# Kernel tuning notes

Measured on AMD Instinct MI355X. Metric: run time of the kernel, lower is better.

## Reference

```python
import jax, jax.numpy as jnp
import numpy as np

D_MODEL = 1024
N_HEADS = 16
HEAD_DIM = D_MODEL // N_HEADS


def setup_inputs() -> dict:
    key = jax.random.key(0)
    ks = jax.random.split(key, 5)
    x = jax.random.normal(ks[0], (4, 2048, D_MODEL), dtype=jnp.float32)
    # Linear weights stored torch-style as (out, in); biases (out,)
    s = 1.0 / np.sqrt(D_MODEL)
    W_qkv = jax.random.uniform(ks[1], (3 * D_MODEL, D_MODEL), jnp.float32, -s, s)
    b_qkv = jax.random.uniform(ks[2], (3 * D_MODEL,), jnp.float32, -s, s)
    W_proj = jax.random.uniform(ks[3], (D_MODEL, D_MODEL), jnp.float32, -s, s)
    b_proj = jax.random.uniform(ks[4], (D_MODEL,), jnp.float32, -s, s)
    return {"x": x, "W_qkv": W_qkv, "b_qkv": b_qkv, "W_proj": W_proj, "b_proj": b_proj}


def reference(x, W_qkv, b_qkv, W_proj, b_proj):
    B, T, C = x.shape
    nh, hs = N_HEADS, HEAD_DIM
    qkv = jnp.einsum('btc,oc->bto', x, W_qkv) + b_qkv  # (B,T,3C)
    q, k, v = jnp.split(qkv, 3, axis=-1)
    # (B, nh, T, hs)
    q = q.reshape(B, T, nh, hs).transpose(0, 2, 1, 3)
    k = k.reshape(B, T, nh, hs).transpose(0, 2, 1, 3)
    v = v.reshape(B, T, nh, hs).transpose(0, 2, 1, 3)
    att = jnp.einsum('bhqd,bhkd->bhqk', q, k) * (hs ** -0.5)  # (B,nh,T,T)
    causal = jnp.tril(jnp.ones((T, T), dtype=bool))
    att = jnp.where(causal[None, None], att, -jnp.inf)
    att = jax.nn.softmax(att, axis=-1)
    y = jnp.einsum('bhqk,bhkd->bhqd', att, v)  # (B,nh,T,hs)
    y = y.transpose(0, 2, 1, 3).reshape(B, T, C)
    y = jnp.einsum('btc,oc->bto', y, W_proj) + b_proj
    return y
```

## Files before the change

kernel.cpp:

```cpp
#include <hip/hip_runtime.h>
#include <math.h>

typedef __bf16 bf16;
typedef __bf16 bf16x4 __attribute__((ext_vector_type(4)));
typedef __bf16 bf16x8 __attribute__((ext_vector_type(8)));
typedef float  f32x4  __attribute__((ext_vector_type(4)));
typedef unsigned short u16;

#define MFMA16(a, b, c) __builtin_amdgcn_mfma_f32_16x16x32_bf16((a), (b), (c), 0, 0, 0)

constexpr int Bz    = 4;
constexpr int Ts    = 2048;
constexpr int DM    = 1024;
constexpr int NH    = 16;
constexpr int HS    = 64;
constexpr int MROWS = Bz * Ts;
constexpr int NQKV  = 3 * DM;

__device__ __forceinline__ unsigned int pack2(bf16 lo, bf16 hi) {
    return ((unsigned int)__builtin_bit_cast(u16, hi) << 16) |
            (unsigned int)__builtin_bit_cast(u16, lo);
}

__device__ __forceinline__ void load_lds16(const bf16* g, bf16* l) {
    __builtin_amdgcn_global_load_lds(
        (__attribute__((address_space(1))) void*)(g),
        (__attribute__((address_space(3))) void*)(l), 16, 0, 0);
}

__global__ void cvt_kernel(const float* __restrict__ in, bf16* __restrict__ out, int n4) {
    int i = blockIdx.x * blockDim.x + threadIdx.x;
    if (i < n4) {
        float4 v = ((const float4*)in)[i];
        bf16x4 o = { (bf16)v.x, (bf16)v.y, (bf16)v.z, (bf16)v.w };
        ((bf16x4*)out)[i] = o;
    }
}

template <int OUT_BF16>
__global__ __launch_bounds__(256) void gemm_bt(const bf16* __restrict__ A,
                                               const bf16* __restrict__ Bw,
                                               const float* __restrict__ bias,
                                               void* __restrict__ Cout,
                                               int M, int N, int K)
{
    __shared__ __align__(16) bf16 As[128 * 32];
    __shared__ __align__(16) bf16 Bs[128 * 32];

    const int tid  = threadIdx.x;
    const int wave = tid >> 6, lane = tid & 63;
    const int quad = lane >> 4, l16 = lane & 15;
    const int wm = (wave >> 1) * 64, wn = (wave & 1) * 64;
    const int m0 = blockIdx.x * 128, n0 = blockIdx.y * 128;

    f32x4 acc[4][4] = {};

    const int c0 = tid, c1 = tid + 256;
    const bf16* gA0 = A  + (size_t)(m0 + (c0 >> 2)) * K + (c0 & 3) * 8;
    const bf16* gA1 = A  + (size_t)(m0 + (c1 >> 2)) * K + (c1 & 3) * 8;
    const bf16* gB0 = Bw + (size_t)(n0 + (c0 >> 2)) * K + (c0 & 3) * 8;
    const bf16* gB1 = Bw + (size_t)(n0 + (c1 >> 2)) * K + (c1 & 3) * 8;
    bf16* lA0 = As + c0 * 8;  bf16* lA1 = As + c1 * 8;
    bf16* lB0 = Bs + c0 * 8;  bf16* lB1 = Bs + c1 * 8;

    for (int kb = 0; kb < K; kb += 32) {
        if (kb) __syncthreads();
        load_lds16(gA0 + kb, lA0);
        load_lds16(gA1 + kb, lA1);
        load_lds16(gB0 + kb, lB0);
        load_lds16(gB1 + kb, lB1);
        __syncthreads();

        bf16x8 af[4], bfr[4];
#pragma unroll
        for (int mt = 0; mt < 4; ++mt)
            af[mt] = *(const bf16x8*)(As + (wm + mt * 16 + l16) * 32 + quad * 8);
#pragma unroll
        for (int nt = 0; nt < 4; ++nt)
            bfr[nt] = *(const bf16x8*)(Bs + (wn + nt * 16 + l16) * 32 + quad * 8);
#pragma unroll
        for (int mt = 0; mt < 4; ++mt)
#pragma unroll
            for (int nt = 0; nt < 4; ++nt)
                acc[mt][nt] = MFMA16(af[mt], bfr[nt], acc[mt][nt]);
    }

#pragma unroll
    for (int mt = 0; mt < 4; ++mt)
#pragma unroll
        for (int nt = 0; nt < 4; ++nt) {
            const int row = m0 + wm + mt * 16 + quad * 4;
            const int col = n0 + wn + nt * 16 + l16;
            const float bc = bias[col];
#pragma unroll
            for (int r = 0; r < 4; ++r) {
                const float v = acc[mt][nt][r] + bc;
                if (OUT_BF16) ((bf16*)Cout)[(size_t)(row + r) * N + col] = (bf16)v;
                else          ((float*)Cout)[(size_t)(row + r) * N + col] = v;
            }
        }
}

__device__ __forceinline__ int vswz(int d) { return ((d ^ (d >> 3)) & 7) << 3; }

__global__ __launch_bounds__(256) void attn_kernel(const bf16* __restrict__ qkv,
                                                   bf16* __restrict__ y)
{
    __shared__ __align__(16) bf16 Ks[64][72];
    __shared__ __align__(16) bf16 Vt[64][72];
    __shared__ __align__(16) bf16 Ps[4][16][72];

    const int p = blockIdx.x, h = blockIdx.y, b = blockIdx.z;
    const int tid  = threadIdx.x;
    const int wave = tid >> 6, lane = tid & 63;
    const int quad = lane >> 4, l16 = lane & 15;

    const bf16* kbase = qkv + (size_t)(b * Ts) * NQKV + DM     + h * HS;
    const bf16* vbase = qkv + (size_t)(b * Ts) * NQKV + 2 * DM + h * HS;

    const int dg = tid & 7, kp = tid >> 3;
    const int k0 = 2 * kp;

    for (int phase = 0; phase < 2; ++phase) {
        const int qt = phase ? (31 - p) : p;
        const int qw = qt * 64 + wave * 16;
        const int q_abs = qw + l16;

        const bf16* qrow = qkv + (size_t)(b * Ts + qw + l16) * NQKV + h * HS;
        const bf16x8 qf0 = *(const bf16x8*)(qrow + quad * 8);
        const bf16x8 qf1 = *(const bf16x8*)(qrow + 32 + quad * 8);

        f32x4 o[4] = {};
        float m_run = -1e30f, l_run = 0.f;

        for (int kt = 0; kt <= qt; ++kt) {
            __syncthreads();

            {
                int e = tid * 8;
#pragma unroll
                for (int rr = 0; rr < 2; ++rr, e += 2048) {
                    const int key = e >> 6, c = e & 63;
                    bf16x8 kv = *(const bf16x8*)(kbase + (size_t)(kt * 64 + key) * NQKV + c);
                    *(bf16x8*)&Ks[key][c] = kv;
                }
            }
            {
                const bf16x8 v0 = *(const bf16x8*)(vbase + (size_t)(kt * 64 + k0)     * NQKV + dg * 8);
                const bf16x8 v1 = *(const bf16x8*)(vbase + (size_t)(kt * 64 + k0 + 1) * NQKV + dg * 8);
#pragma unroll
                for (int j = 0; j < 8; ++j) {
                    const int d = dg * 8 + j;
                    *(unsigned int*)&Vt[d][k0 ^ vswz(d)] = pack2(v0[j], v1[j]);
                }
            }
            __syncthreads();

            f32x4 s[4];
#pragma unroll
            for (int sub = 0; sub < 4; ++sub) {
                bf16x8 kf0 = *(const bf16x8*)&Ks[sub * 16 + l16][quad * 8];
                bf16x8 kf1 = *(const bf16x8*)&Ks[sub * 16 + l16][32 + quad * 8];
                f32x4 z = {};
                z = MFMA16(kf0, qf0, z);
                z = MFMA16(kf1, qf1, z);
                s[sub] = z;
            }

#pragma unroll
            for (int sub = 0; sub < 4; ++sub) {
                const int kb = kt * 64 + sub * 16 + quad * 4;
#pragma unroll
                for (int r = 0; r < 4; ++r)
                    s[sub][r] = (kb + r <= q_abs) ? s[sub][r] * 0.125f : -1e30f;
            }

            float mx = -1e30f;
#pragma unroll
            for (int sub = 0; sub < 4; ++sub)
#pragma unroll
                for (int r = 0; r < 4; ++r) mx = fmaxf(mx, s[sub][r]);
            mx = fmaxf(mx, __shfl_xor(mx, 16, 64));
            mx = fmaxf(mx, __shfl_xor(mx, 32, 64));
            const float mnew  = fmaxf(m_run, mx);
            const float alpha = __expf(m_run - mnew);
            float ls = 0.f;
#pragma unroll
            for (int sub = 0; sub < 4; ++sub)
#pragma unroll
                for (int r = 0; r < 4; ++r) {
                    const float pv = __expf(s[sub][r] - mnew);
                    s[sub][r] = pv;
                    ls += pv;
                }
            ls += __shfl_xor(ls, 16, 64);
            ls += __shfl_xor(ls, 32, 64);
            l_run = l_run * alpha + ls;
            m_run = mnew;
#pragma unroll
            for (int dt = 0; dt < 4; ++dt)
#pragma unroll
                for (int r = 0; r < 4; ++r) o[dt][r] *= alpha;

#pragma unroll
            for (int sub = 0; sub < 4; ++sub) {
                const int kc = sub * 16 + quad * 4;
                *(unsigned int*)&Ps[wave][l16][kc]     = pack2((bf16)s[sub][0], (bf16)s[sub][1]);
                *(unsigned int*)&Ps[wave][l16][kc + 2] = pack2((bf16)s[sub][2], (bf16)s[sub][3]);
            }
            __asm__ volatile("" ::: "memory");

            bf16x8 pb0 = *(const bf16x8*)&Ps[wave][l16][quad * 8];
            bf16x8 pb1 = *(const bf16x8*)&Ps[wave][l16][32 + quad * 8];

#pragma unroll
            for (int kb = 0; kb < 2; ++kb) {
                const int kcol = kb * 32 + quad * 8;
#pragma unroll
                for (int dt = 0; dt < 4; ++dt) {
                    const int d = dt * 16 + l16;
                    bf16x8 vf = *(const bf16x8*)&Vt[d][kcol ^ vswz(d)];
                    o[dt] = MFMA16(vf, kb ? pb1 : pb0, o[dt]);
                }
            }
        }

        const float inv = 1.f / l_run;
        bf16* yrow = y + (size_t)(b * Ts + qw + l16) * DM + h * HS;
#pragma unroll
        for (int dt = 0; dt < 4; ++dt) {
            bf16x4 ov;
#pragma unroll
            for (int r = 0; r < 4; ++r) ov[r] = (bf16)(o[dt][r] * inv);
            *(bf16x4*)(yrow + dt * 16 + quad * 4) = ov;
        }
    }
}

extern "C" void kernel_launch(void* const* d_in, const int* in_sizes, int n_in,
                              void* d_out, int out_size, void* d_ws, size_t ws_size,
                              hipStream_t stream)
{
    const float* x     = (const float*)d_in[0];
    const float* Wqkv  = (const float*)d_in[1];
    const float* bqkv  = (const float*)d_in[2];
    const float* Wproj = (const float*)d_in[3];
    const float* bproj = (const float*)d_in[4];

    char* ws = (char*)d_ws;
    bf16* xb     = (bf16*)ws;  ws += (size_t)MROWS * DM * 2;
    bf16* wqkvb  = (bf16*)ws;  ws += (size_t)NQKV * DM * 2;
    bf16* wprojb = (bf16*)ws;  ws += (size_t)DM * DM * 2;
    bf16* qkvb   = (bf16*)ws;  ws += (size_t)MROWS * NQKV * 2;
    bf16* yb     = (bf16*)ws;

    cvt_kernel<<<MROWS * DM / 4 / 256, 256, 0, stream>>>(x, xb, MROWS * DM / 4);
    cvt_kernel<<<NQKV * DM / 4 / 256, 256, 0, stream>>>(Wqkv, wqkvb, NQKV * DM / 4);
    cvt_kernel<<<DM * DM / 4 / 256, 256, 0, stream>>>(Wproj, wprojb, DM * DM / 4);

    gemm_bt<1><<<dim3(MROWS / 128, NQKV / 128), 256, 0, stream>>>(
        xb, wqkvb, bqkv, qkvb, MROWS, NQKV, DM);

    attn_kernel<<<dim3(16, NH, Bz), 256, 0, stream>>>(qkvb, yb);

    gemm_bt<0><<<dim3(MROWS / 128, DM / 128), 256, 0, stream>>>(
        yb, wprojb, bproj, d_out, MROWS, DM, DM);
}
```

Before: 280.3 us.

## Fold softmax scale into QKV GEMM, use exp2, and peel the causal-mask tile

The QKV GEMM epilogue now multiplies the Q columns by 0.125*log2(e), so the attention kernel can call the hardware exp2 directly and skip the per-element scale. The key-tile loop becomes a lambda: only the diagonal tile applies the causal mask, and the max and sum reductions become balanced trees. The V-transpose swizzle is also simplified, which may change LDS bank-conflict behaviour. Q is now rounded to bf16 after scaling, which adds a slight precision difference.

```diff
diff --git a/kernel.cpp b/kernel.cpp
--- a/kernel.cpp
+++ b/kernel.cpp
@@ -17,6 +17,8 @@
 constexpr int MROWS = Bz * Ts;
 constexpr int NQKV  = 3 * DM;
 
+#define QSCALE 0.18033688011112042f
+
 __device__ __forceinline__ unsigned int pack2(bf16 lo, bf16 hi) {
     return ((unsigned int)__builtin_bit_cast(u16, hi) << 16) |
             (unsigned int)__builtin_bit_cast(u16, lo);
@@ -42,7 +44,8 @@
                                                const bf16* __restrict__ Bw,
                                                const float* __restrict__ bias,
                                                void* __restrict__ Cout,
-                                               int M, int N, int K)
+                                               int M, int N, int K,
+                                               float qscale, int qcols)
 {
     __shared__ __align__(16) bf16 As[128 * 32];
     __shared__ __align__(16) bf16 Bs[128 * 32];
@@ -92,16 +95,17 @@
             const int row = m0 + wm + mt * 16 + quad * 4;
             const int col = n0 + wn + nt * 16 + l16;
             const float bc = bias[col];
+            const float sc = (col < qcols) ? qscale : 1.0f;
 #pragma unroll
             for (int r = 0; r < 4; ++r) {
-                const float v = acc[mt][nt][r] + bc;
+                const float v = (acc[mt][nt][r] + bc) * sc;
                 if (OUT_BF16) ((bf16*)Cout)[(size_t)(row + r) * N + col] = (bf16)v;
                 else          ((float*)Cout)[(size_t)(row + r) * N + col] = v;
             }
         }
 }
 
-__device__ __forceinline__ int vswz(int d) { return ((d ^ (d >> 3)) & 7) << 3; }
+__device__ __forceinline__ int vswz(int d) { return ((d >> 3) & 7) << 3; }
 
 __global__ __launch_bounds__(256) void attn_kernel(const bf16* __restrict__ qkv,
                                                    bf16* __restrict__ y)
@@ -133,7 +137,7 @@
         f32x4 o[4] = {};
         float m_run = -1e30f, l_run = 0.f;
 
-        for (int kt = 0; kt <= qt; ++kt) {
+        auto iter = [&](int kt, bool masked) {
             __syncthreads();
 
             {
@@ -167,32 +171,35 @@
                 s[sub] = z;
             }
 
-#pragma unroll
-            for (int sub = 0; sub < 4; ++sub) {
-                const int kb = kt * 64 + sub * 16 + quad * 4;
-#pragma unroll
-                for (int r = 0; r < 4; ++r)
-                    s[sub][r] = (kb + r <= q_abs) ? s[sub][r] * 0.125f : -1e30f;
-            }
-
-            float mx = -1e30f;
-#pragma unroll
-            for (int sub = 0; sub < 4; ++sub)
-#pragma unroll
-                for (int r = 0; r < 4; ++r) mx = fmaxf(mx, s[sub][r]);
+            if (masked) {
+#pragma unroll
+                for (int sub = 0; sub < 4; ++sub) {
+                    const int kb = kt * 64 + sub * 16 + quad * 4;
+#pragma unroll
+                    for (int r = 0; r < 4; ++r)
+                        if (kb + r > q_abs) s[sub][r] = -1e30f;
+                }
+            }
+
+            float mA = fmaxf(fmaxf(s[0][0], s[0][1]), fmaxf(s[0][2], s[0][3]));
+            float mB = fmaxf(fmaxf(s[1][0], s[1][1]), fmaxf(s[1][2], s[1][3]));
+            float mC = fmaxf(fmaxf(s[2][0], s[2][1]), fmaxf(s[2][2], s[2][3]));
+            float mD = fmaxf(fmaxf(s[3][0], s[3][1]), fmaxf(s[3][2], s[3][3]));
+            float mx = fmaxf(fmaxf(mA, mB), fmaxf(mC, mD));
             mx = fmaxf(mx, __shfl_xor(mx, 16, 64));
             mx = fmaxf(mx, __shfl_xor(mx, 32, 64));
             const float mnew  = fmaxf(m_run, mx);
-            const float alpha = __expf(m_run - mnew);
-            float ls = 0.f;
+            const float alpha = __builtin_amdgcn_exp2f(m_run - mnew);
 #pragma unroll
             for (int sub = 0; sub < 4; ++sub)
 #pragma unroll
-                for (int r = 0; r < 4; ++r) {
-                    const float pv = __expf(s[sub][r] - mnew);
-                    s[sub][r] = pv;
-                    ls += pv;
-                }
+                for (int r = 0; r < 4; ++r)
+                    s[sub][r] = __builtin_amdgcn_exp2f(s[sub][r] - mnew);
+            float t0 = (s[0][0] + s[0][1]) + (s[0][2] + s[0][3]);
+            float t1 = (s[1][0] + s[1][1]) + (s[1][2] + s[1][3]);
+            float t2 = (s[2][0] + s[2][1]) + (s[2][2] + s[2][3]);
+            float t3 = (s[3][0] + s[3][1]) + (s[3][2] + s[3][3]);
+            float ls = (t0 + t1) + (t2 + t3);
             ls += __shfl_xor(ls, 16, 64);
             ls += __shfl_xor(ls, 32, 64);
             l_run = l_run * alpha + ls;
@@ -223,7 +230,10 @@
                     o[dt] = MFMA16(vf, kb ? pb1 : pb0, o[dt]);
                 }
             }
-        }
+        };
+
+        for (int kt = 0; kt < qt; ++kt) iter(kt, false);
+        iter(qt, true);
 
         const float inv = 1.f / l_run;
         bf16* yrow = y + (size_t)(b * Ts + qw + l16) * DM + h * HS;
@@ -259,10 +269,10 @@
     cvt_kernel<<<DM * DM / 4 / 256, 256, 0, stream>>>(Wproj, wprojb, DM * DM / 4);
 
     gemm_bt<1><<<dim3(MROWS / 128, NQKV / 128), 256, 0, stream>>>(
-        xb, wqkvb, bqkv, qkvb, MROWS, NQKV, DM);
+        xb, wqkvb, bqkv, qkvb, MROWS, NQKV, DM, QSCALE, DM);
 
     attn_kernel<<<dim3(16, NH, Bz), 256, 0, stream>>>(qkvb, yb);
 
     gemm_bt<0><<<dim3(MROWS / 128, DM / 128), 256, 0, stream>>>(
-        yb, wprojb, bproj, d_out, MROWS, DM, DM);
-}
+        yb, wprojb, bproj, d_out, MROWS, DM, DM, 1.0f, 0);
+}
```

Result: faster. 274.8 us (-2.0%).
